# Performance work log

Measured on AMD Instinct MI355X. Metric: run time of the kernel, lower is better.

Reference implementation:

```python
import jax, jax.numpy as jnp
import numpy as np

DIM = 768
HEADS = 12
HIDDEN = 3072
EPS = 1e-5


def _layernorm(x, g, b):
    mu = jnp.mean(x, axis=-1, keepdims=True)
    var = jnp.var(x, axis=-1, keepdims=True)
    return (x - mu) * jax.lax.rsqrt(var + EPS) * g + b


def setup_inputs() -> dict:
    key = jax.random.key(0)
    ks = jax.random.split(key, 10)
    s_in = 1.0 / np.sqrt(DIM)
    s_hid = 1.0 / np.sqrt(HIDDEN)
    return {
        "x": jax.random.normal(ks[0], (8, 1024, DIM), dtype=jnp.float32),
        "ln1_g": jnp.ones((DIM,), jnp.float32),
        "ln1_b": jnp.zeros((DIM,), jnp.float32),
        "qkv_w": jax.random.uniform(ks[1], (DIM, 3 * DIM), jnp.float32, -s_in, s_in),
        "qkv_b": jnp.zeros((3 * DIM,), jnp.float32),
        "proj_w": jax.random.uniform(ks[2], (DIM, DIM), jnp.float32, -s_in, s_in),
        "proj_b": jnp.zeros((DIM,), jnp.float32),
        "ln2_g": jnp.ones((DIM,), jnp.float32),
        "ln2_b": jnp.zeros((DIM,), jnp.float32),
        "fc1_w": jax.random.uniform(ks[3], (DIM, HIDDEN), jnp.float32, -s_in, s_in),
        "fc1_b": jnp.zeros((HIDDEN,), jnp.float32),
        "fc2_w": jax.random.uniform(ks[4], (HIDDEN, DIM), jnp.float32, -s_hid, s_hid),
        "fc2_b": jnp.zeros((DIM,), jnp.float32),
    }


def reference(x, ln1_g, ln1_b, qkv_w, qkv_b, proj_w, proj_b,
              ln2_g, ln2_b, fc1_w, fc1_b, fc2_w, fc2_b):
    B, N, C = x.shape
    H = HEADS
    Dh = C // H
    scale = Dh ** -0.5

    # --- attention sublayer (pre-norm) ---
    h = _layernorm(x, ln1_g, ln1_b)
    qkv = h @ qkv_w + qkv_b  # [B,N,3C]
    qkv = qkv.reshape(B, N, 3, H, Dh)
    q = qkv[:, :, 0].transpose(0, 2, 1, 3)  # [B,H,N,Dh]
    k = qkv[:, :, 1].transpose(0, 2, 1, 3)
    v = qkv[:, :, 2].transpose(0, 2, 1, 3)
    attn = jax.nn.softmax(jnp.einsum('bhnd,bhmd->bhnm', q, k) * scale, axis=-1)
    o = jnp.einsum('bhnm,bhmd->bhnd', attn, v)  # [B,H,N,Dh]
    o = o.transpose(0, 2, 1, 3).reshape(B, N, C)
    x = x + (o @ proj_w + proj_b)

    # --- MLP sublayer (pre-norm) ---
    h = _layernorm(x, ln2_g, ln2_b)
    h = jax.nn.gelu(h @ fc1_w + fc1_b, approximate=False)
    x = x + (h @ fc2_w + fc2_b)
    return x
```

## Files before the change

kernel.cpp:

```cpp
#include <hip/hip_runtime.h>
#include <math.h>

#define DIM    768
#define HEADS  12
#define HIDDEN 3072
#define SEQ    1024
#define NTOK   8192
#define QKVLD  2304

typedef __bf16 bf16_t;
typedef __bf16 bf16x4 __attribute__((ext_vector_type(4)));
typedef __bf16 bf16x8 __attribute__((ext_vector_type(8)));
typedef float  f32x4  __attribute__((ext_vector_type(4)));

union ABFrag { bf16x4 h[2]; bf16x8 v; };

__device__ __forceinline__ void gload16(const void* g, void* l) {
  __builtin_amdgcn_global_load_lds(
      (const __attribute__((address_space(1))) void*)g,
      (__attribute__((address_space(3))) void*)l, 16, 0, 0);
}

__device__ __forceinline__ f32x4 mfma16(bf16x8 a, bf16x8 b, f32x4 c) {
  return __builtin_amdgcn_mfma_f32_16x16x32_bf16(a, b, c, 0, 0, 0);
}

__device__ __forceinline__ ABFrag load_frag(const bf16_t* rowp, int g) {
  ABFrag f;
  f.h[0] = *(const bf16x4*)(rowp + 4 * g);
  f.h[1] = *(const bf16x4*)(rowp + 4 * g + 16);
  return f;
}

__device__ __forceinline__ ABFrag load_frag_swz(const bf16_t* base, int row, int e, int g) {
  const int o0 = e + 4 * g, o1 = o0 + 16;
  const int s = row & 7;
  const bf16_t* rp = base + row * 64;
  ABFrag f;
  f.h[0] = *(const bf16x4*)(rp + ((((o0 >> 3) ^ s) << 3) | (o0 & 7)));
  f.h[1] = *(const bf16x4*)(rp + ((((o1 >> 3) ^ s) << 3) | (o1 & 7)));
  return f;
}

__device__ __forceinline__ bf16x8 ldsfrag(const bf16_t* base, int row, int lc) {
  return *(const bf16x8*)(base + row * 64 + ((lc ^ (row & 7)) << 3));
}

__device__ __forceinline__ float gelu_f(float v) {
  float u = v * fmaf(v * v, 0.0356774081f, 0.7978845608f);
  u = fminf(u, 15.0f);
  float t = __builtin_amdgcn_exp2f(u * 2.8853900817779268f);
  return v * t * __builtin_amdgcn_rcpf(t + 1.0f);
}

__global__ __launch_bounds__(256) void ln_kernel(
    const float* __restrict__ x, const float* __restrict__ gw,
    const float* __restrict__ bw, bf16_t* __restrict__ out) {
  const int row = blockIdx.x;
  const int t = threadIdx.x;
  const float* xr = x + (size_t)row * DIM;
  float v0 = xr[t], v1 = xr[t + 256], v2 = xr[t + 512];
  float s = v0 + v1 + v2;
  float s2 = v0 * v0 + v1 * v1 + v2 * v2;
  #pragma unroll
  for (int o = 32; o > 0; o >>= 1) {
    s += __shfl_down(s, o);
    s2 += __shfl_down(s2, o);
  }
  __shared__ float red[8];
  if ((t & 63) == 0) { red[(t >> 6) * 2] = s; red[(t >> 6) * 2 + 1] = s2; }
  __syncthreads();
  float S  = red[0] + red[2] + red[4] + red[6];
  float S2 = red[1] + red[3] + red[5] + red[7];
  float mu  = S * (1.0f / DIM);
  float var = S2 * (1.0f / DIM) - mu * mu;
  float rs  = rsqrtf(var + 1e-5f);
  bf16_t* orow = out + (size_t)row * DIM;
  orow[t]       = (bf16_t)((v0 - mu) * rs * gw[t]       + bw[t]);
  orow[t + 256] = (bf16_t)((v1 - mu) * rs * gw[t + 256] + bw[t + 256]);
  orow[t + 512] = (bf16_t)((v2 - mu) * rs * gw[t + 512] + bw[t + 512]);
}

__global__ __launch_bounds__(256) void wtrans_kernel(
    const float* __restrict__ W, bf16_t* __restrict__ Wt, int K, int N) {
  __shared__ float tile[32][33];
  const int tx = threadIdx.x, ty = threadIdx.y;
  const int n0 = blockIdx.x * 32, k0 = blockIdx.y * 32;
  #pragma unroll
  for (int i = 0; i < 4; ++i)
    tile[ty + i * 8][tx] = W[(size_t)(k0 + ty + i * 8) * N + n0 + tx];
  __syncthreads();
  #pragma unroll
  for (int i = 0; i < 4; ++i)
    Wt[(size_t)(n0 + ty + i * 8) * K + k0 + tx] = (bf16_t)tile[tx][ty + i * 8];
}

__global__ __launch_bounds__(256) void vtrans_kernel(
    const bf16_t* __restrict__ qkv, bf16_t* __restrict__ vt) {
  __shared__ bf16_t tile[64][65];
  const int bh = blockIdx.y, b = bh / HEADS, h = bh % HEADS;
  const int n0 = blockIdx.x * 64;
  const int t = threadIdx.x;
  const int c = t & 63, rr = t >> 6;
  const bf16_t* src = qkv + (size_t)(b * SEQ + n0) * QKVLD + 2 * DIM + h * 64;
  #pragma unroll
  for (int i = 0; i < 16; ++i)
    tile[c][rr + i * 4] = src[(size_t)(rr + i * 4) * QKVLD + c];
  __syncthreads();
  bf16_t* dst = vt + (size_t)bh * 64 * SEQ + n0;
  #pragma unroll
  for (int i = 0; i < 16; ++i)
    dst[(size_t)(rr + i * 4) * SEQ + c] = tile[rr + i * 4][c];
}

template <int MODE>
__global__ __launch_bounds__(256) void gemm_sb(
    const bf16_t* __restrict__ A, const bf16_t* __restrict__ Bt,
    int N, int K,
    const float* __restrict__ bias, const float* __restrict__ res,
    void* __restrict__ outv, int gx) {
  __shared__ bf16_t sA[128 * 64];
  __shared__ bf16_t sB[128 * 64];
  const int tid = threadIdx.x;
  const int lane = tid & 63;
  const int wid = tid >> 6;
  const int g = lane >> 4, r16 = lane & 15;

  const int nwg = gridDim.x;
  const int cpx = nwg >> 3;
  const int sw = (blockIdx.x & 7) * cpx + (blockIdx.x >> 3);
  const int bx = sw % gx, by = sw / gx;
  const int row0 = by * 128, col0 = bx * 128;
  const int wr = (wid >> 1) * 64, wc = (wid & 1) * 64;

  f32x4 acc[4][4];
  #pragma unroll
  for (int m = 0; m < 4; ++m)
    #pragma unroll
    for (int n = 0; n < 4; ++n) acc[m][n] = f32x4{0.f, 0.f, 0.f, 0.f};

  const int kSteps = K >> 6;
  for (int kt = 0; kt < kSteps; ++kt) {
    __syncthreads();
    #pragma unroll
    for (int rnd = 0; rnd < 4; ++rnd) {
      const int c = rnd * 256 + tid;
      const int row = c >> 3, scp = (c & 7) ^ (row & 7);
      gload16(A + (size_t)(row0 + row) * K + (size_t)kt * 64 + scp * 8, &sA[c * 8]);
    }
    #pragma unroll
    for (int rnd = 0; rnd < 4; ++rnd) {
      const int c = rnd * 256 + tid;
      const int row = c >> 3, scp = (c & 7) ^ (row & 7);
      gload16(Bt + (size_t)(col0 + row) * K + (size_t)kt * 64 + scp * 8, &sB[c * 8]);
    }
    __syncthreads();
    bf16x8 af[4][2], bfr[4][2];
    #pragma unroll
    for (int m = 0; m < 4; ++m)
      #pragma unroll
      for (int kk = 0; kk < 2; ++kk)
        af[m][kk] = ldsfrag(sA, wr + m * 16 + r16, kk * 4 + g);
    #pragma unroll
    for (int n = 0; n < 4; ++n)
      #pragma unroll
      for (int kk = 0; kk < 2; ++kk)
        bfr[n][kk] = ldsfrag(sB, wc + n * 16 + r16, kk * 4 + g);
    #pragma unroll
    for (int kk = 0; kk < 2; ++kk)
      #pragma unroll
      for (int m = 0; m < 4; ++m)
        #pragma unroll
        for (int n = 0; n < 4; ++n)
          acc[m][n] = mfma16(af[m][kk], bfr[n][kk], acc[m][n]);
  }

  #pragma unroll
  for (int m = 0; m < 4; ++m) {
    const int rowb = row0 + wr + m * 16 + 4 * g;
    #pragma unroll
    for (int n = 0; n < 4; ++n) {
      const int col = col0 + wc + n * 16 + r16;
      const float bv = bias[col];
      #pragma unroll
      for (int r = 0; r < 4; ++r) {
        const size_t idx = (size_t)(rowb + r) * N + col;
        float v = acc[m][n][r] + bv;
        if (MODE == 0) {
          ((bf16_t*)outv)[idx] = (bf16_t)v;
        } else if (MODE == 1) {
          ((float*)outv)[idx] = v + res[idx];
        } else {
          ((bf16_t*)outv)[idx] = (bf16_t)gelu_f(v);
        }
      }
    }
  }
}

template <int MODE>
__global__ __launch_bounds__(256) void gemm_db(
    const bf16_t* __restrict__ A, const bf16_t* __restrict__ Bt,
    int N, int K,
    const float* __restrict__ bias, const float* __restrict__ res,
    void* __restrict__ outv, int gx) {
  __shared__ bf16_t sA[2][128 * 64];
  __shared__ bf16_t sB[2][128 * 64];
  const int tid = threadIdx.x;
  const int lane = tid & 63;
  const int wid = tid >> 6;
  const int g = lane >> 4, r16 = lane & 15;

  const int nwg = gridDim.x;
  const int cpx = nwg >> 3;
  const int sw = (blockIdx.x & 7) * cpx + (blockIdx.x >> 3);
  const int bx = sw % gx, by = sw / gx;
  const int row0 = by * 128, col0 = bx * 128;
  const int wr = (wid >> 1) * 64, wc = (wid & 1) * 64;

  auto stage = [&](int p, int kt) {
    #pragma unroll
    for (int rnd = 0; rnd < 4; ++rnd) {
      const int c = rnd * 256 + tid;
      const int row = c >> 3, scp = (c & 7) ^ (row & 7);
      gload16(A + (size_t)(row0 + row) * K + (size_t)kt * 64 + scp * 8,
              &sA[p][c * 8]);
    }
    #pragma unroll
    for (int rnd = 0; rnd < 4; ++rnd) {
      const int c = rnd * 256 + tid;
      const int row = c >> 3, scp = (c & 7) ^ (row & 7);
      gload16(Bt + (size_t)(col0 + row) * K + (size_t)kt * 64 + scp * 8,
              &sB[p][c * 8]);
    }
  };

  f32x4 acc[4][4];
  #pragma unroll
  for (int m = 0; m < 4; ++m)
    #pragma unroll
    for (int n = 0; n < 4; ++n) acc[m][n] = f32x4{0.f, 0.f, 0.f, 0.f};

  const int kSteps = K >> 6;
  stage(0, 0);
  for (int kt = 0; kt < kSteps; ++kt) {
    const int cur = kt & 1;
    __syncthreads();
    if (kt + 1 < kSteps) stage(cur ^ 1, kt + 1);

    bf16x8 af[4][2], bfr[4][2];
    #pragma unroll
    for (int m = 0; m < 4; ++m)
      #pragma unroll
      for (int kk = 0; kk < 2; ++kk)
        af[m][kk] = ldsfrag(&sA[cur][0], wr + m * 16 + r16, kk * 4 + g);
    #pragma unroll
    for (int n = 0; n < 4; ++n)
      #pragma unroll
      for (int kk = 0; kk < 2; ++kk)
        bfr[n][kk] = ldsfrag(&sB[cur][0], wc + n * 16 + r16, kk * 4 + g);
    #pragma unroll
    for (int kk = 0; kk < 2; ++kk)
      #pragma unroll
      for (int m = 0; m < 4; ++m)
        #pragma unroll
        for (int n = 0; n < 4; ++n)
          acc[m][n] = mfma16(af[m][kk], bfr[n][kk], acc[m][n]);
  }

  #pragma unroll
  for (int m = 0; m < 4; ++m) {
    const int rowb = row0 + wr + m * 16 + 4 * g;
    #pragma unroll
    for (int n = 0; n < 4; ++n) {
      const int col = col0 + wc + n * 16 + r16;
      const float bv = bias[col];
      #pragma unroll
      for (int r = 0; r < 4; ++r) {
        const size_t idx = (size_t)(rowb + r) * N + col;
        float v = acc[m][n][r] + bv;
        if (MODE == 0) {
          ((bf16_t*)outv)[idx] = (bf16_t)v;
        } else if (MODE == 1) {
          ((float*)outv)[idx] = v + res[idx];
        } else {
          ((bf16_t*)outv)[idx] = (bf16_t)gelu_f(v);
        }
      }
    }
  }
}

__global__ __launch_bounds__(512) void attn_kernel(
    const bf16_t* __restrict__ qkv, const bf16_t* __restrict__ vt,
    bf16_t* __restrict__ o) {
  __shared__ bf16_t kbuf[2][64 * 64];
  __shared__ bf16_t vbuf[2][64 * 64];
  const int bh = blockIdx.y, b = bh / HEADS, h = bh % HEADS;
  const int q0 = blockIdx.x * 128;
  const int tid = threadIdx.x, lane = tid & 63, wid = tid >> 6;
  const int g = lane >> 4, r16 = lane & 15;

  const bf16_t* qptr = qkv + (size_t)b * SEQ * QKVLD + h * 64;
  const bf16_t* kptr = qptr + DIM;
  const bf16_t* vtp  = vt + (size_t)bh * 64 * SEQ;

  ABFrag aq[2];
  {
    const bf16_t* qr = qptr + (size_t)(q0 + wid * 16 + r16) * QKVLD;
    aq[0] = load_frag(qr, g);
    aq[1] = load_frag(qr + 32, g);
  }

  float lacc = 0.f;
  f32x4 acco[4];
  #pragma unroll
  for (int n = 0; n < 4; ++n) acco[n] = f32x4{0.f, 0.f, 0.f, 0.f};

  auto stage = [&](int buf, int kv0) {
    const int row = tid >> 3, scp = (tid & 7) ^ (row & 7);
    gload16(kptr + (size_t)(kv0 + row) * QKVLD + scp * 8, &kbuf[buf][tid * 8]);
    gload16(vtp + (size_t)row * SEQ + kv0 + scp * 8, &vbuf[buf][tid * 8]);
  };

  const float C2 = 0.125f * 1.4426950408889634f;

  stage(0, 0);
  for (int it = 0; it < SEQ / 64; ++it) {
    const int cur = it & 1;
    __syncthreads();
    if (it + 1 < SEQ / 64) stage(cur ^ 1, (it + 1) * 64);

    f32x4 st[4];
    __builtin_amdgcn_s_setprio(1);
    #pragma unroll
    for (int t = 0; t < 4; ++t) {
      st[t] = f32x4{0.f, 0.f, 0.f, 0.f};
      ABFrag ak0 = load_frag_swz(kbuf[cur], t * 16 + r16, 0, g);
      st[t] = mfma16(ak0.v, aq[0].v, st[t]);
      ABFrag ak1 = load_frag_swz(kbuf[cur], t * 16 + r16, 32, g);
      st[t] = mfma16(ak1.v, aq[1].v, st[t]);
    }
    __builtin_amdgcn_s_setprio(0);

    float p[4][4];
    #pragma unroll
    for (int t = 0; t < 4; ++t)
      #pragma unroll
      for (int r = 0; r < 4; ++r) {
        float e = __builtin_amdgcn_exp2f(fmaf(st[t][r], C2, -16.0f));
        p[t][r] = e;
        lacc += e;
      }

    ABFrag pa0, pa1;
    #pragma unroll
    for (int r = 0; r < 4; ++r) {
      pa0.h[0][r] = (bf16_t)p[0][r];
      pa0.h[1][r] = (bf16_t)p[1][r];
      pa1.h[0][r] = (bf16_t)p[2][r];
      pa1.h[1][r] = (bf16_t)p[3][r];
    }

    __builtin_amdgcn_s_setprio(1);
    #pragma unroll
    for (int n = 0; n < 4; ++n) {
      ABFrag bv0 = load_frag_swz(vbuf[cur], n * 16 + r16, 0, g);
      acco[n] = mfma16(pa0.v, bv0.v, acco[n]);
      ABFrag bv1 = load_frag_swz(vbuf[cur], n * 16 + r16, 32, g);
      acco[n] = mfma16(pa1.v, bv1.v, acco[n]);
    }
    __builtin_amdgcn_s_setprio(0);
  }

  float lt = lacc;
  lt += __shfl_xor(lt, 16);
  lt += __shfl_xor(lt, 32);
  float linv[4];
  #pragma unroll
  for (int r = 0; r < 4; ++r) linv[r] = 1.0f / __shfl(lt, 4 * g + r);
  bf16_t* op = o + (size_t)(b * SEQ + q0 + wid * 16 + 4 * g) * DIM + h * 64;
  #pragma unroll
  for (int n = 0; n < 4; ++n)
    #pragma unroll
    for (int r = 0; r < 4; ++r)
      op[(size_t)r * DIM + n * 16 + r16] = (bf16_t)(acco[n][r] * linv[r]);
}

extern "C" void kernel_launch(void* const* d_in, const int* in_sizes, int n_in,
                              void* d_out, int out_size, void* d_ws, size_t ws_size,
                              hipStream_t stream) {
  const float* x      = (const float*)d_in[0];
  const float* ln1_g  = (const float*)d_in[1];
  const float* ln1_b  = (const float*)d_in[2];
  const float* qkv_w  = (const float*)d_in[3];
  const float* qkv_b  = (const float*)d_in[4];
  const float* proj_w = (const float*)d_in[5];
  const float* proj_b = (const float*)d_in[6];
  const float* ln2_g  = (const float*)d_in[7];
  const float* ln2_b  = (const float*)d_in[8];
  const float* fc1_w  = (const float*)d_in[9];
  const float* fc1_b  = (const float*)d_in[10];
  const float* fc2_w  = (const float*)d_in[11];
  const float* fc2_b  = (const float*)d_in[12];
  float* out = (float*)d_out;

  char* ws = (char*)d_ws;
  size_t off = 0;
  auto alloc = [&](size_t bytes) -> void* {
    void* p = ws + off;
    off += (bytes + 255) & ~(size_t)255;
    return p;
  };
  bf16_t* wqkvT  = (bf16_t*)alloc((size_t)QKVLD * DIM * 2);
  bf16_t* wprojT = (bf16_t*)alloc((size_t)DIM * DIM * 2);
  bf16_t* wfc1T  = (bf16_t*)alloc((size_t)HIDDEN * DIM * 2);
  bf16_t* wfc2T  = (bf16_t*)alloc((size_t)DIM * HIDDEN * 2);
  bf16_t* buf1   = (bf16_t*)alloc((size_t)NTOK * DIM * 2);
  bf16_t* buf2   = (bf16_t*)alloc((size_t)NTOK * HIDDEN * 2);
  bf16_t* buf3   = (bf16_t*)alloc((size_t)NTOK * DIM * 2);
  float*  x1     = (float*)alloc((size_t)NTOK * DIM * 4);

  bf16_t* h1 = buf1;     bf16_t* obf = buf1;
  bf16_t* qkvbf = buf2;  bf16_t* h3 = buf2;
  bf16_t* vt = buf3;     bf16_t* h2 = buf3;
  (void)in_sizes; (void)n_in; (void)out_size; (void)ws_size;

  dim3 tb(32, 8);
  wtrans_kernel<<<dim3(QKVLD / 32, DIM / 32), tb, 0, stream>>>(qkv_w, wqkvT, DIM, QKVLD);
  wtrans_kernel<<<dim3(DIM / 32, DIM / 32), tb, 0, stream>>>(proj_w, wprojT, DIM, DIM);
  wtrans_kernel<<<dim3(HIDDEN / 32, DIM / 32), tb, 0, stream>>>(fc1_w, wfc1T, DIM, HIDDEN);
  wtrans_kernel<<<dim3(DIM / 32, HIDDEN / 32), tb, 0, stream>>>(fc2_w, wfc2T, HIDDEN, DIM);

  ln_kernel<<<NTOK, 256, 0, stream>>>(x, ln1_g, ln1_b, h1);
  gemm_sb<0><<<(QKVLD / 128) * (NTOK / 128), 256, 0, stream>>>(
      h1, wqkvT, QKVLD, DIM, qkv_b, nullptr, qkvbf, QKVLD / 128);
  vtrans_kernel<<<dim3(SEQ / 64, 8 * HEADS), 256, 0, stream>>>(qkvbf, vt);
  attn_kernel<<<dim3(SEQ / 128, 8 * HEADS), 512, 0, stream>>>(qkvbf, vt, obf);
  gemm_db<1><<<(DIM / 128) * (NTOK / 128), 256, 0, stream>>>(
      obf, wprojT, DIM, DIM, proj_b, x, x1, DIM / 128);
  ln_kernel<<<NTOK, 256, 0, stream>>>(x1, ln2_g, ln2_b, h2);
  gemm_sb<2><<<(HIDDEN / 128) * (NTOK / 128), 256, 0, stream>>>(
      h2, wfc1T, HIDDEN, DIM, fc1_b, nullptr, h3, HIDDEN / 128);
  gemm_db<1><<<(DIM / 128) * (NTOK / 128), 256, 0, stream>>>(
      h3, wfc2T, DIM, HIDDEN, fc2_b, x1, out, DIM / 128);
}
```

Before: 263.1 us.

## Vectorize layernorm per-wave rows, hoist attention LDS offsets, swap attention grid axes

LayerNorm now handles one row per wavefront with float4 loads and bf16x4 stores, which removes the shared-memory reduction and the block barrier and cuts the block count by four. The attention kernel precomputes its swizzled LDS fragment offsets and staging source pointers once instead of recomputing them every iteration. It also swaps the grid axes so blocks for the same (batch, head) are no longer adjacent, which changes scheduling order and K/V cache locality. The trade-off is more registers held for the offset table and a possible loss of L2 reuse of K/V across neighbouring blocks.

```diff
diff --git a/kernel.cpp b/kernel.cpp
--- a/kernel.cpp
+++ b/kernel.cpp
@@ -32,16 +32,6 @@
   return f;
 }
 
-__device__ __forceinline__ ABFrag load_frag_swz(const bf16_t* base, int row, int e, int g) {
-  const int o0 = e + 4 * g, o1 = o0 + 16;
-  const int s = row & 7;
-  const bf16_t* rp = base + row * 64;
-  ABFrag f;
-  f.h[0] = *(const bf16x4*)(rp + ((((o0 >> 3) ^ s) << 3) | (o0 & 7)));
-  f.h[1] = *(const bf16x4*)(rp + ((((o1 >> 3) ^ s) << 3) | (o1 & 7)));
-  return f;
-}
-
 __device__ __forceinline__ bf16x8 ldsfrag(const bf16_t* base, int row, int lc) {
   return *(const bf16x8*)(base + row * 64 + ((lc ^ (row & 7)) << 3));
 }
@@ -56,29 +46,37 @@
 __global__ __launch_bounds__(256) void ln_kernel(
     const float* __restrict__ x, const float* __restrict__ gw,
     const float* __restrict__ bw, bf16_t* __restrict__ out) {
-  const int row = blockIdx.x;
-  const int t = threadIdx.x;
+  const int row = blockIdx.x * 4 + (threadIdx.x >> 6);
+  const int lane = threadIdx.x & 63;
   const float* xr = x + (size_t)row * DIM;
-  float v0 = xr[t], v1 = xr[t + 256], v2 = xr[t + 512];
-  float s = v0 + v1 + v2;
-  float s2 = v0 * v0 + v1 * v1 + v2 * v2;
+  f32x4 v[3];
+  float s = 0.f, s2 = 0.f;
+  #pragma unroll
+  for (int i = 0; i < 3; ++i) {
+    v[i] = *(const f32x4*)(xr + lane * 4 + i * 256);
+    #pragma unroll
+    for (int j = 0; j < 4; ++j) { s += v[i][j]; s2 += v[i][j] * v[i][j]; }
+  }
   #pragma unroll
   for (int o = 32; o > 0; o >>= 1) {
-    s += __shfl_down(s, o);
-    s2 += __shfl_down(s2, o);
-  }
-  __shared__ float red[8];
-  if ((t & 63) == 0) { red[(t >> 6) * 2] = s; red[(t >> 6) * 2 + 1] = s2; }
-  __syncthreads();
-  float S  = red[0] + red[2] + red[4] + red[6];
-  float S2 = red[1] + red[3] + red[5] + red[7];
-  float mu  = S * (1.0f / DIM);
-  float var = S2 * (1.0f / DIM) - mu * mu;
-  float rs  = rsqrtf(var + 1e-5f);
+    s += __shfl_xor(s, o);
+    s2 += __shfl_xor(s2, o);
+  }
+  const float mu  = s * (1.0f / DIM);
+  const float var = s2 * (1.0f / DIM) - mu * mu;
+  const float rs  = rsqrtf(var + 1e-5f);
   bf16_t* orow = out + (size_t)row * DIM;
-  orow[t]       = (bf16_t)((v0 - mu) * rs * gw[t]       + bw[t]);
-  orow[t + 256] = (bf16_t)((v1 - mu) * rs * gw[t + 256] + bw[t + 256]);
-  orow[t + 512] = (bf16_t)((v2 - mu) * rs * gw[t + 512] + bw[t + 512]);
+  #pragma unroll
+  for (int i = 0; i < 3; ++i) {
+    const int c = lane * 4 + i * 256;
+    f32x4 gv = *(const f32x4*)(gw + c);
+    f32x4 bv = *(const f32x4*)(bw + c);
+    bf16x4 o4;
+    #pragma unroll
+    for (int j = 0; j < 4; ++j)
+      o4[j] = (bf16_t)((v[i][j] - mu) * rs * gv[j] + bv[j]);
+    *(bf16x4*)(orow + c) = o4;
+  }
 }
 
 __global__ __launch_bounds__(256) void wtrans_kernel(
@@ -296,8 +294,8 @@
     bf16_t* __restrict__ o) {
   __shared__ bf16_t kbuf[2][64 * 64];
   __shared__ bf16_t vbuf[2][64 * 64];
-  const int bh = blockIdx.y, b = bh / HEADS, h = bh % HEADS;
-  const int q0 = blockIdx.x * 128;
+  const int bh = blockIdx.x, b = bh / HEADS, h = bh % HEADS;
+  const int q0 = blockIdx.y * 128;
   const int tid = threadIdx.x, lane = tid & 63, wid = tid >> 6;
   const int g = lane >> 4, r16 = lane & 15;
 
@@ -312,15 +310,29 @@
     aq[1] = load_frag(qr + 32, g);
   }
 
+  int off[4][2][2];
+  #pragma unroll
+  for (int i = 0; i < 4; ++i) {
+    const int row = i * 16 + r16, s = row & 7, rp = row * 64;
+    #pragma unroll
+    for (int e2 = 0; e2 < 2; ++e2) {
+      const int o0 = e2 * 32 + 4 * g, o1 = o0 + 16;
+      off[i][e2][0] = rp + ((((o0 >> 3) ^ s) << 3) | (o0 & 7));
+      off[i][e2][1] = rp + ((((o1 >> 3) ^ s) << 3) | (o1 & 7));
+    }
+  }
+
   float lacc = 0.f;
   f32x4 acco[4];
   #pragma unroll
   for (int n = 0; n < 4; ++n) acco[n] = f32x4{0.f, 0.f, 0.f, 0.f};
 
+  const int srow = tid >> 3, sscp = (tid & 7) ^ (srow & 7);
+  const bf16_t* kSrc = kptr + (size_t)srow * QKVLD + sscp * 8;
+  const bf16_t* vSrc = vtp + (size_t)srow * SEQ + sscp * 8;
   auto stage = [&](int buf, int kv0) {
-    const int row = tid >> 3, scp = (tid & 7) ^ (row & 7);
-    gload16(kptr + (size_t)(kv0 + row) * QKVLD + scp * 8, &kbuf[buf][tid * 8]);
-    gload16(vtp + (size_t)row * SEQ + kv0 + scp * 8, &vbuf[buf][tid * 8]);
+    gload16(kSrc + (size_t)kv0 * QKVLD, &kbuf[buf][tid * 8]);
+    gload16(vSrc + kv0, &vbuf[buf][tid * 8]);
   };
 
   const float C2 = 0.125f * 1.4426950408889634f;
@@ -330,15 +342,20 @@
     const int cur = it & 1;
     __syncthreads();
     if (it + 1 < SEQ / 64) stage(cur ^ 1, (it + 1) * 64);
+    const bf16_t* kb = kbuf[cur];
+    const bf16_t* vb = vbuf[cur];
 
     f32x4 st[4];
     __builtin_amdgcn_s_setprio(1);
     #pragma unroll
     for (int t = 0; t < 4; ++t) {
       st[t] = f32x4{0.f, 0.f, 0.f, 0.f};
-      ABFrag ak0 = load_frag_swz(kbuf[cur], t * 16 + r16, 0, g);
+      ABFrag ak0, ak1;
+      ak0.h[0] = *(const bf16x4*)(kb + off[t][0][0]);
+      ak0.h[1] = *(const bf16x4*)(kb + off[t][0][1]);
       st[t] = mfma16(ak0.v, aq[0].v, st[t]);
-      ABFrag ak1 = load_frag_swz(kbuf[cur], t * 16 + r16, 32, g);
+      ak1.h[0] = *(const bf16x4*)(kb + off[t][1][0]);
+      ak1.h[1] = *(const bf16x4*)(kb + off[t][1][1]);
       st[t] = mfma16(ak1.v, aq[1].v, st[t]);
     }
     __builtin_amdgcn_s_setprio(0);
@@ -365,9 +382,12 @@
     __builtin_amdgcn_s_setprio(1);
     #pragma unroll
     for (int n = 0; n < 4; ++n) {
-      ABFrag bv0 = load_frag_swz(vbuf[cur], n * 16 + r16, 0, g);
+      ABFrag bv0, bv1;
+      bv0.h[0] = *(const bf16x4*)(vb + off[n][0][0]);
+      bv0.h[1] = *(const bf16x4*)(vb + off[n][0][1]);
       acco[n] = mfma16(pa0.v, bv0.v, acco[n]);
-      ABFrag bv1 = load_frag_swz(vbuf[cur], n * 16 + r16, 32, g);
+      bv1.h[0] = *(const bf16x4*)(vb + off[n][1][0]);
+      bv1.h[1] = *(const bf16x4*)(vb + off[n][1][1]);
       acco[n] = mfma16(pa1.v, bv1.v, acco[n]);
     }
     __builtin_amdgcn_s_setprio(0);
@@ -432,14 +452,14 @@
   wtrans_kernel<<<dim3(HIDDEN / 32, DIM / 32), tb, 0, stream>>>(fc1_w, wfc1T, DIM, HIDDEN);
   wtrans_kernel<<<dim3(DIM / 32, HIDDEN / 32), tb, 0, stream>>>(fc2_w, wfc2T, HIDDEN, DIM);
 
-  ln_kernel<<<NTOK, 256, 0, stream>>>(x, ln1_g, ln1_b, h1);
+  ln_kernel<<<NTOK / 4, 256, 0, stream>>>(x, ln1_g, ln1_b, h1);
   gemm_sb<0><<<(QKVLD / 128) * (NTOK / 128), 256, 0, stream>>>(
       h1, wqkvT, QKVLD, DIM, qkv_b, nullptr, qkvbf, QKVLD / 128);
   vtrans_kernel<<<dim3(SEQ / 64, 8 * HEADS), 256, 0, stream>>>(qkvbf, vt);
-  attn_kernel<<<dim3(SEQ / 128, 8 * HEADS), 512, 0, stream>>>(qkvbf, vt, obf);
+  attn_kernel<<<dim3(8 * HEADS, SEQ / 128), 512, 0, stream>>>(qkvbf, vt, obf);
   gemm_db<1><<<(DIM / 128) * (NTOK / 128), 256, 0, stream>>>(
       obf, wprojT, DIM, DIM, proj_b, x, x1, DIM / 128);
-  ln_kernel<<<NTOK, 256, 0, stream>>>(x1, ln2_g, ln2_b, h2);
+  ln_kernel<<<NTOK / 4, 256, 0, stream>>>(x1, ln2_g, ln2_b, h2);
   gemm_sb<2><<<(HIDDEN / 128) * (NTOK / 128), 256, 0, stream>>>(
       h2, wfc1T, HIDDEN, DIM, fc1_b, nullptr, h3, HIDDEN / 128);
   gemm_db<1><<<(DIM / 128) * (NTOK / 128), 256, 0, stream>>>(
```

New measurement: 256.2 us. -2.6%, faster.
